# Kernel optimization log

Measured on AMD Instinct MI355X. Metric: run time of the kernel, lower is better.

The kernel has to match this reference:

```python
import jax, jax.numpy as jnp
import numpy as np

# Graph/block sizes: 2-hop sampled minibatch
N0, N1, N2 = 655360, 81920, 8192   # src nodes layer0, dst0/src1, dst1 (seeds)
FAN0, FAN1 = 8, 10
E0, E1 = N1 * FAN0, N2 * FAN1       # 655360, 81920
F_IN, H = 128, 256
BN_EPS = 1e-5
L2_EPS = 1e-12


def setup_inputs() -> dict:
    key = jax.random.key(0)
    ks = jax.random.split(key, 16)
    s = 0.05  # param scale
    inp = {
        "x": jax.random.normal(ks[0], (N0, F_IN), jnp.float32),
        "edge_src0": jax.random.randint(ks[1], (E0,), 0, N0, jnp.int32),
        "edge_dst0": jnp.repeat(jnp.arange(N1, dtype=jnp.int32), FAN0),
        "edge_src1": jax.random.randint(ks[2], (E1,), 0, N1, jnp.int32),
        "edge_dst1": jnp.repeat(jnp.arange(N2, dtype=jnp.int32), FAN1),
        "W_pool0": jax.random.normal(ks[3], (F_IN, F_IN), jnp.float32) * s,
        "b_pool0": jnp.zeros((F_IN,), jnp.float32),
        "W_self0": jax.random.normal(ks[4], (F_IN, H), jnp.float32) * s,
        "W_neigh0": jax.random.normal(ks[5], (F_IN, H), jnp.float32) * s,
        "b0": jnp.zeros((H,), jnp.float32),
        "W_pool1": jax.random.normal(ks[6], (H, H), jnp.float32) * s,
        "b_pool1": jnp.zeros((H,), jnp.float32),
        "W_self1": jax.random.normal(ks[7], (H, H), jnp.float32) * s,
        "W_neigh1": jax.random.normal(ks[8], (H, H), jnp.float32) * s,
        "b1": jnp.zeros((H,), jnp.float32),
        "g_bn0": jnp.ones((H,), jnp.float32),
        "be_bn0": jnp.zeros((H,), jnp.float32),
        "W_h": jax.random.normal(ks[9], (H, H), jnp.float32) * s,
        "b_h": jnp.zeros((H,), jnp.float32),
        "g_bnh": jnp.ones((H,), jnp.float32),
        "be_bnh": jnp.zeros((H,), jnp.float32),
        "W_lat": jax.random.normal(ks[10], (H, H), jnp.float32) * s,
        "b_lat": jnp.zeros((H,), jnp.float32),
        "g_bnl": jnp.ones((H,), jnp.float32),
        "be_bnl": jnp.zeros((H,), jnp.float32),
    }
    return inp


def _sage_pool(h, esrc, edst, n_dst, Wp, bp, Ws, Wn, b):
    # DGL SAGEConv aggregator_type='pool':
    # m = relu(fc_pool(h_src)); pooled[v] = max_{u in N(v)} m[u]
    # out = fc_self(h_dst) + fc_neigh(pooled) + bias
    m = jax.nn.relu(h @ Wp + bp)                                  # [N_src, d]
    pooled = jax.ops.segment_max(m[esrc], edst, num_segments=n_dst)
    return h[:n_dst] @ Ws + pooled @ Wn + b


def _l2norm(h):
    n = jnp.sqrt(jnp.sum(h * h, axis=1, keepdims=True))
    return h / jnp.maximum(n, L2_EPS)


def _bn(h, g, b):
    mu = jnp.mean(h, axis=0)
    var = jnp.var(h, axis=0)
    return (h - mu) * jax.lax.rsqrt(var + BN_EPS) * g + b


def reference(x, edge_src0, edge_dst0, edge_src1, edge_dst1,
              W_pool0, b_pool0, W_self0, W_neigh0, b0,
              W_pool1, b_pool1, W_self1, W_neigh1, b1,
              g_bn0, be_bn0, W_h, b_h, g_bnh, be_bnh,
              W_lat, b_lat, g_bnl, be_bnl):
    # layer 0
    h = _sage_pool(x, edge_src0, edge_dst0, N1, W_pool0, b_pool0, W_self0, W_neigh0, b0)
    h = _l2norm(h)
    h = jax.nn.relu(_bn(h, g_bn0, be_bn0))
    # dropout: eval mode (identity)
    h = jax.nn.relu(_bn(h @ W_h + b_h, g_bnh, be_bnh))   # self.hidden
    # layer 1 (last conv)
    h = _sage_pool(h, edge_src1, edge_dst1, N2, W_pool1, b_pool1, W_self1, W_neigh1, b1)
    h = _l2norm(h)
    # self.latent
    h = _bn(h @ W_lat + b_lat, g_bnl, be_bnl)
    return h
```

## Files before the change

kernel.cpp:

```cpp
#include <hip/hip_runtime.h>

typedef unsigned short u16;
typedef unsigned int u32;
typedef float f32x4 __attribute__((ext_vector_type(4)));
typedef int i32x4 __attribute__((ext_vector_type(4)));
typedef __bf16 bf16x8 __attribute__((ext_vector_type(8)));
typedef short s16x8 __attribute__((ext_vector_type(8)));

#define CN0 655360
#define CN1 81920
#define CN2 8192

#define H0_OFF    0ull
#define T_OFF     41943040ull
#define H2_OFF    83886080ull
#define ZZ_OFF    88080384ull
#define WP0F_OFF  96468992ull
#define WC0F_OFF  96501760ull
#define WHF_OFF   96632832ull
#define WP1F_OFF  96763904ull
#define WC1F_OFF  96894976ull
#define WLATF_OFF 97157120ull
#define STAT_OFF  97288192ull

__device__ inline u16 f2bf(float f) {
  u32 u = __builtin_bit_cast(u32, f);
  return (u16)((u + 0x7fffu + ((u >> 16) & 1u)) >> 16);
}
__device__ inline float bf2f(u16 s) {
  return __builtin_bit_cast(float, (u32)s << 16);
}
__device__ inline i32x4 cvt8(f32x4 a, f32x4 b) {
  union { bf16x8 v; i32x4 q; } u;
  #pragma unroll
  for (int j = 0; j < 4; ++j) { u.v[j] = (__bf16)a[j]; u.v[4 + j] = (__bf16)b[j]; }
  return u.q;
}

template <typename V>
__device__ inline auto mfma_sel(V a, V b, f32x4 c, int)
    -> decltype(__builtin_amdgcn_mfma_f32_16x16x32_bf16(a, b, c, 0, 0, 0)) {
  return __builtin_amdgcn_mfma_f32_16x16x32_bf16(a, b, c, 0, 0, 0);
}
template <typename V>
__device__ inline f32x4 mfma_sel(V a, V b, f32x4 c, long) {
  return __builtin_amdgcn_mfma_f32_16x16x32_bf16(
      __builtin_bit_cast(s16x8, a), __builtin_bit_cast(s16x8, b), c, 0, 0, 0);
}
__device__ inline f32x4 MFMA(i32x4 a, i32x4 b, f32x4 c) {
  return mfma_sel(__builtin_bit_cast(bf16x8, a), __builtin_bit_cast(bf16x8, b), c, 0);
}

__device__ void fragify(const float* W0, const float* W1, int Khalf, int N,
                        u16* dst, int tid, int nthr) {
  int K = W1 ? 2 * Khalf : Khalf;
  int ntile = N >> 4;
  int total = (K >> 5) * ntile * 512;
  for (int i = tid; i < total; i += nthr) {
    int j = i & 7;
    int lane = (i >> 3) & 63;
    int nt = (i >> 9) % ntile;
    int kt = i / (512 * ntile);
    int k = kt * 32 + ((lane >> 4) << 3) + j;
    int n = nt * 16 + (lane & 15);
    float v = (k < Khalf) ? W0[k * N + n] : W1[(k - Khalf) * N + n];
    dst[i] = f2bf(v);
  }
}

__global__ void kprep(const float* Wp0, const float* Ws0, const float* Wn0,
                      const float* Wh, const float* Wp1, const float* Ws1,
                      const float* Wn1, const float* Wlat,
                      u16* wp0f, u16* wc0f, u16* whf, u16* wp1f, u16* wc1f,
                      u16* wlatf, float* stat) {
  int tid = blockIdx.x * blockDim.x + threadIdx.x;
  int nthr = gridDim.x * blockDim.x;
  if (blockIdx.x == 0) {
    #pragma unroll
    for (int i = 0; i < 6; ++i) stat[threadIdx.x + i * 256] = 0.0f;
  }
  fragify(Wp0, nullptr, 128, 128, wp0f, tid, nthr);
  fragify(Ws0, Wn0, 128, 256, wc0f, tid, nthr);
  fragify(Wh, nullptr, 256, 256, whf, tid, nthr);
  fragify(Wp1, nullptr, 256, 256, wp1f, tid, nthr);
  fragify(Ws1, Wn1, 256, 256, wc1f, tid, nthr);
  fragify(Wlat, nullptr, 256, 256, wlatf, tid, nthr);
}

__global__ __launch_bounds__(256, 4)
void k1_layer0(const float* __restrict__ x, const int* __restrict__ esrc,
               const u16* __restrict__ wp0f, const u16* __restrict__ wc0f,
               const float* __restrict__ bp0, const float* __restrict__ b0v,
               u16* __restrict__ h0, float* __restrict__ stat0) {
  __shared__ __align__(16) char lds[16896];
  float* rsb = (float*)(lds + 16384);
  int tid = threadIdx.x, lane = tid & 63, w = tid >> 6;
  int r15 = lane & 15, g = lane >> 4;
  int d0 = blockIdx.x * 32;

  int i_ = tid >> 3, part_ = tid & 7;
  const float* xr_ = x + (size_t)(d0 + i_) * 128 + part_ * 16;
  f32x4 t0 = *(const f32x4*)(xr_ + 0);
  f32x4 t1 = *(const f32x4*)(xr_ + 4);
  f32x4 t2 = *(const f32x4*)(xr_ + 8);
  f32x4 t3 = *(const f32x4*)(xr_ + 12);

  {
    int e0 = d0 * 8 + w * 64;
    const float* rp[4];
    #pragma unroll
    for (int rt = 0; rt < 4; ++rt)
      rp[rt] = x + (size_t)esrc[e0 + rt * 16 + r15] * 128;
    i32x4 afr[4][4];
    #pragma unroll
    for (int rt = 0; rt < 4; ++rt)
      #pragma unroll
      for (int kt = 0; kt < 4; ++kt) {
        f32x4 p0 = *(const f32x4*)(rp[rt] + kt * 32 + g * 8);
        f32x4 p1 = *(const f32x4*)(rp[rt] + kt * 32 + g * 8 + 4);
        afr[rt][kt] = cvt8(p0, p1);
      }
    for (int nt = 0; nt < 8; ++nt) {
      f32x4 acc[4] = {};
      #pragma unroll
      for (int kt = 0; kt < 4; ++kt) {
        i32x4 b = *(const i32x4*)(wp0f + (((kt * 8 + nt) * 64 + lane) << 3));
        #pragma unroll
        for (int rt = 0; rt < 4; ++rt) acc[rt] = MFMA(afr[rt][kt], b, acc[rt]);
      }
      float bias = bp0[nt * 16 + r15];
      #pragma unroll
      for (int rt = 0; rt < 4; ++rt) {
        float mx = fmaxf(fmaxf(acc[rt][0], acc[rt][1]), fmaxf(acc[rt][2], acc[rt][3]));
        mx = fmaxf(mx + bias, 0.0f);
        mx = fmaxf(mx, __shfl_xor(mx, 16));
        if ((g & 1) == 0) {
          u32 row = (u32)(w * 8 + rt * 2 + (g >> 1));
          u32 byte = (row * 512 + 256 + (u32)(nt * 16 + r15) * 2) ^ ((row & 7) << 4);
          *(u16*)(lds + byte) = f2bf(mx);
        }
      }
    }
  }

  {
    u32 sw = (u32)((i_ & 7) << 4);
    *(i32x4*)(lds + (((u32)i_ * 512 + (u32)part_ * 32) ^ sw)) = cvt8(t0, t1);
    *(i32x4*)(lds + (((u32)i_ * 512 + (u32)part_ * 32 + 16) ^ sw)) = cvt8(t2, t3);
  }
  __syncthreads();

  f32x4 acc2[4][2] = {};
  for (int kt = 0; kt < 8; ++kt) {
    u32 r0 = (u32)r15, r1 = (u32)(16 + r15);
    i32x4 a0 = *(const i32x4*)(lds + ((r0 * 512 + (u32)kt * 64 + (u32)g * 16) ^ ((r0 & 7) << 4)));
    i32x4 a1 = *(const i32x4*)(lds + ((r1 * 512 + (u32)kt * 64 + (u32)g * 16) ^ ((r1 & 7) << 4)));
    #pragma unroll
    for (int n4 = 0; n4 < 4; ++n4) {
      int nt = w * 4 + n4;
      i32x4 b = *(const i32x4*)(wc0f + (((size_t)(kt * 16 + nt) * 64 + lane) << 3));
      acc2[n4][0] = MFMA(a0, b, acc2[n4][0]);
      acc2[n4][1] = MFMA(a1, b, acc2[n4][1]);
    }
  }

  float vn[4][2][4];
  #pragma unroll
  for (int n4 = 0; n4 < 4; ++n4) {
    float bv = b0v[(w * 4 + n4) * 16 + r15];
    #pragma unroll
    for (int rt = 0; rt < 2; ++rt)
      #pragma unroll
      for (int j = 0; j < 4; ++j) vn[n4][rt][j] = acc2[n4][rt][j] + bv;
  }
  #pragma unroll
  for (int rt = 0; rt < 2; ++rt)
    #pragma unroll
    for (int j = 0; j < 4; ++j) {
      float s = 0.0f;
      #pragma unroll
      for (int n4 = 0; n4 < 4; ++n4) s += vn[n4][rt][j] * vn[n4][rt][j];
      s += __shfl_xor(s, 1); s += __shfl_xor(s, 2);
      s += __shfl_xor(s, 4); s += __shfl_xor(s, 8);
      if (r15 == 0) rsb[(rt * 16 + g * 4 + j) * 4 + w] = s;
    }
  __syncthreads();

  #pragma unroll
  for (int rt = 0; rt < 2; ++rt)
    #pragma unroll
    for (int j = 0; j < 4; ++j) {
      int r = rt * 16 + g * 4 + j;
      f32x4 q = *(const f32x4*)&rsb[r * 4];
      float rn = 1.0f / fmaxf(sqrtf(q[0] + q[1] + q[2] + q[3]), 1e-12f);
      #pragma unroll
      for (int n4 = 0; n4 < 4; ++n4) vn[n4][rt][j] *= rn;
    }
  #pragma unroll
  for (int n4 = 0; n4 < 4; ++n4) {
    int col = (w * 4 + n4) * 16 + r15;
    float s1 = 0.0f, s2 = 0.0f;
    #pragma unroll
    for (int rt = 0; rt < 2; ++rt)
      #pragma unroll
      for (int j = 0; j < 4; ++j) { float v = vn[n4][rt][j]; s1 += v; s2 += v * v; }
    s1 += __shfl_xor(s1, 16); s1 += __shfl_xor(s1, 32);
    s2 += __shfl_xor(s2, 16); s2 += __shfl_xor(s2, 32);
    if (g == 0) { atomicAdd(&stat0[col], s1); atomicAdd(&stat0[256 + col], s2); }
  }
  #pragma unroll
  for (int n4 = 0; n4 < 4; ++n4)
    #pragma unroll
    for (int rt = 0; rt < 2; ++rt)
      #pragma unroll
      for (int j = 0; j < 4; ++j)
        *(u16*)(lds + (u32)(rt * 16 + g * 4 + j) * 512 + (u32)((w * 4 + n4) * 16 + r15) * 2)
            = f2bf(vn[n4][rt][j]);
  __syncthreads();
  {
    int i = tid >> 3, c8 = tid & 7;
    const char* srcp = lds + i * 512 + c8 * 64;
    u16* dst = h0 + (size_t)(d0 + i) * 256 + c8 * 32;
    #pragma unroll
    for (int c = 0; c < 4; ++c)
      *(i32x4*)(dst + c * 8) = *(const i32x4*)(srcp + c * 16);
  }
}

template <bool RELU_OUT, bool STATS, bool H2OUT>
__global__ __launch_bounds__(256, 4)
void gemm64(const u16* __restrict__ Ain, const float* __restrict__ statin,
            float inv_n, const float* __restrict__ gg, const float* __restrict__ bb,
            const u16* __restrict__ Bf, const float* __restrict__ bias,
            u16* __restrict__ Out, float* __restrict__ statout,
            u16* __restrict__ H2out) {
  __shared__ __align__(16) char lds[34816];
  u16* tb = (u16*)lds;
  float* scs = (float*)(lds + 32768);
  int tid = threadIdx.x, lane = tid & 63, w = tid >> 6;
  int r15 = lane & 15, g = lane >> 4;
  int d0 = blockIdx.x * 64;
  {
    float mu = statin[tid] * inv_n;
    float var = statin[256 + tid] * inv_n - mu * mu;
    float sc = gg[tid] / sqrtf(var + 1e-5f);
    scs[tid] = sc;
    scs[256 + tid] = bb[tid] - mu * sc;
  }
  __syncthreads();

  {
    int i = tid >> 2, part = tid & 3;
    const u16* ar = Ain + (size_t)(d0 + i) * 256 + part * 64;
    u32 sw = (u32)((i & 7) << 4), rowb = (u32)i * 512;
    for (int cc = 0; cc < 8; ++cc) {
      union { i32x4 q; u16 h[8]; } in, out;
      in.q = *(const i32x4*)(ar + cc * 8);
      #pragma unroll
      for (int j = 0; j < 8; ++j) {
        int k = part * 64 + cc * 8 + j;
        float v = fmaxf(bf2f(in.h[j]) * scs[k] + scs[256 + k], 0.0f);
        out.h[j] = f2bf(v);
      }
      *(i32x4*)(lds + ((rowb + (u32)(part * 64 + cc * 8) * 2) ^ sw)) = out.q;
    }
  }
  __syncthreads();

  f32x4 acc[4][4] = {};
  for (int kt = 0; kt < 8; ++kt) {
    i32x4 a[4];
    #pragma unroll
    for (int rt = 0; rt < 4; ++rt) {
      u32 r = (u32)(rt * 16 + r15);
      a[rt] = *(const i32x4*)(lds + ((r * 512 + (u32)kt * 64 + (u32)g * 16) ^ ((r & 7) << 4)));
    }
    #pragma unroll
    for (int n4 = 0; n4 < 4; ++n4) {
      int nt = w * 4 + n4;
      i32x4 b = *(const i32x4*)(Bf + (((size_t)(kt * 16 + nt) * 64 + lane) << 3));
      #pragma unroll
      for (int rt = 0; rt < 4; ++rt) acc[n4][rt] = MFMA(a[rt], b, acc[n4][rt]);
    }
  }
  __syncthreads();

  if constexpr (H2OUT) {
    if (d0 < CN2) {
      int i = tid >> 2, part = tid & 3;
      u16* orow = H2out + (size_t)(d0 + i) * 256 + part * 64;
      u32 sw = (u32)((i & 7) << 4);
      #pragma unroll
      for (int cc = 0; cc < 8; ++cc)
        *(i32x4*)(orow + cc * 8) =
            *(const i32x4*)(lds + (((u32)i * 512 + (u32)(part * 64 + cc * 8) * 2) ^ sw));
    }
    __syncthreads();
  }

  #pragma unroll
  for (int n4 = 0; n4 < 4; ++n4) {
    int col = (w * 4 + n4) * 16 + r15;
    float bv = bias[col];
    #pragma unroll
    for (int rt = 0; rt < 4; ++rt)
      #pragma unroll
      for (int j = 0; j < 4; ++j) {
        float v = acc[n4][rt][j] + bv;
        if (RELU_OUT) v = fmaxf(v, 0.0f);
        tb[(rt * 16 + g * 4 + j) * 256 + col] = f2bf(v);
      }
  }
  __syncthreads();

  {
    int i = tid >> 2, part = tid & 3;
    u16* orow = Out + (size_t)(d0 + i) * 256 + part * 64;
    const u16* trow = tb + i * 256 + part * 64;
    #pragma unroll
    for (int cc = 0; cc < 8; ++cc)
      *(i32x4*)(orow + cc * 8) = *(const i32x4*)(trow + cc * 8);
  }
  if (STATS) {
    int c = tid; float s1 = 0.0f, s2 = 0.0f;
    for (int r = 0; r < 64; ++r) { float v = bf2f(tb[r * 256 + c]); s1 += v; s2 += v * v; }
    atomicAdd(&statout[c], s1); atomicAdd(&statout[256 + c], s2);
  }
}

__global__ __launch_bounds__(256, 4)
void k6_layer1(const int* __restrict__ esrc1, const u16* __restrict__ m1,
               const u16* __restrict__ h2, const u16* __restrict__ wc1f,
               const u16* __restrict__ wlatf, const float* __restrict__ b1v,
               const float* __restrict__ blat, float* __restrict__ zz,
               float* __restrict__ statl) {
  __shared__ __align__(16) char lds[40960];
  float* zbuf = (float*)(lds + 16384);
  int tid = threadIdx.x, lane = tid & 63, w = tid >> 6;
  int r15 = lane & 15, g = lane >> 4;
  int d0 = blockIdx.x * 16;

  {
    int i = tid >> 4, part = tid & 15;
    u32 sw = (u32)((i & 7) << 4);
    const u16* hrow = h2 + (size_t)(d0 + i) * 256 + part * 16;
    i32x4 q0 = *(const i32x4*)(hrow);
    i32x4 q1 = *(const i32x4*)(hrow + 8);
    *(i32x4*)(lds + (((u32)i * 1024 + (u32)(part * 16) * 2) ^ sw)) = q0;
    *(i32x4*)(lds + (((u32)i * 1024 + (u32)(part * 16) * 2 + 16) ^ sw)) = q1;
    float mx[16];
    #pragma unroll
    for (int c = 0; c < 16; ++c) mx[c] = -1e30f;
    const int* ep = esrc1 + (d0 + i) * 10;
    #pragma unroll 2
    for (int e = 0; e < 10; ++e) {
      int src = ep[e];
      const u16* mrow = m1 + (size_t)src * 256 + part * 16;
      union { i32x4 q; u16 h[8]; } a, b;
      a.q = *(const i32x4*)(mrow);
      b.q = *(const i32x4*)(mrow + 8);
      #pragma unroll
      for (int j = 0; j < 8; ++j) {
        mx[j] = fmaxf(mx[j], bf2f(a.h[j]));
        mx[8 + j] = fmaxf(mx[8 + j], bf2f(b.h[j]));
      }
    }
    union { i32x4 q; u16 h[8]; } p0, p1;
    #pragma unroll
    for (int j = 0; j < 8; ++j) { p0.h[j] = f2bf(mx[j]); p1.h[j] = f2bf(mx[8 + j]); }
    *(i32x4*)(lds + (((u32)i * 1024 + (u32)(256 + part * 16) * 2) ^ sw)) = p0.q;
    *(i32x4*)(lds + (((u32)i * 1024 + (u32)(256 + part * 16) * 2 + 16) ^ sw)) = p1.q;
  }
  __syncthreads();

  {
    f32x4 acc[4] = {};
    for (int kt = 0; kt < 16; ++kt) {
      u32 r0 = (u32)r15;
      i32x4 a0 = *(const i32x4*)(lds + ((r0 * 1024 + (u32)kt * 64 + (u32)g * 16) ^ ((r0 & 7) << 4)));
      #pragma unroll
      for (int n4 = 0; n4 < 4; ++n4) {
        int nt = w * 4 + n4;
        i32x4 b = *(const i32x4*)(wc1f + (((size_t)(kt * 16 + nt) * 64 + lane) << 3));
        acc[n4] = MFMA(a0, b, acc[n4]);
      }
    }
    #pragma unroll
    for (int n4 = 0; n4 < 4; ++n4) {
      int col = (w * 4 + n4) * 16 + r15;
      float bv = b1v[col];
      #pragma unroll
      for (int j = 0; j < 4; ++j)
        zbuf[(g * 4 + j) * 256 + col] = acc[n4][j] + bv;
    }
  }
  __syncthreads();

  {
    int i = tid >> 4, part = tid & 15;
    float* zr = zbuf + i * 256 + part * 16;
    f32x4 v0 = *(const f32x4*)(zr + 0), v1 = *(const f32x4*)(zr + 4);
    f32x4 v2 = *(const f32x4*)(zr + 8), v3 = *(const f32x4*)(zr + 12);
    float ss = 0.0f;
    #pragma unroll
    for (int j = 0; j < 4; ++j) ss += v0[j]*v0[j] + v1[j]*v1[j] + v2[j]*v2[j] + v3[j]*v3[j];
    ss += __shfl_xor(ss, 1); ss += __shfl_xor(ss, 2);
    ss += __shfl_xor(ss, 4); ss += __shfl_xor(ss, 8);
    float rn = 1.0f / fmaxf(sqrtf(ss), 1e-12f);
    v0 *= rn; v1 *= rn; v2 *= rn; v3 *= rn;
    u32 sw = (u32)((i & 7) << 4);
    *(i32x4*)(lds + 32768 + (((u32)i * 512 + (u32)(part * 16) * 2) ^ sw)) = cvt8(v0, v1);
    *(i32x4*)(lds + 32768 + (((u32)i * 512 + (u32)(part * 16) * 2 + 16) ^ sw)) = cvt8(v2, v3);
  }
  __syncthreads();

  {
    f32x4 acc[4] = {};
    for (int kt = 0; kt < 8; ++kt) {
      u32 r0 = (u32)r15;
      i32x4 a0 = *(const i32x4*)(lds + 32768 + ((r0 * 512 + (u32)kt * 64 + (u32)g * 16) ^ ((r0 & 7) << 4)));
      #pragma unroll
      for (int n4 = 0; n4 < 4; ++n4) {
        int nt = w * 4 + n4;
        i32x4 b = *(const i32x4*)(wlatf + (((size_t)(kt * 16 + nt) * 64 + lane) << 3));
        acc[n4] = MFMA(a0, b, acc[n4]);
      }
    }
    #pragma unroll
    for (int n4 = 0; n4 < 4; ++n4) {
      int col = (w * 4 + n4) * 16 + r15;
      float bv = blat[col];
      #pragma unroll
      for (int j = 0; j < 4; ++j)
        zbuf[(g * 4 + j) * 256 + col] = acc[n4][j] + bv;
    }
  }
  __syncthreads();

  {
    int i = tid >> 4, part = tid & 15;
    float* zr = zbuf + i * 256 + part * 16;
    float* orow = zz + (size_t)(d0 + i) * 256 + part * 16;
    #pragma unroll
    for (int c = 0; c < 16; c += 4) *(f32x4*)(orow + c) = *(const f32x4*)(zr + c);
  }
  {
    int c = tid; float s1 = 0.0f, s2 = 0.0f;
    #pragma unroll
    for (int r = 0; r < 16; ++r) { float v = zbuf[r * 256 + c]; s1 += v; s2 += v * v; }
    atomicAdd(&statl[c], s1); atomicAdd(&statl[256 + c], s2);
  }
}

__global__ void k7_out(const float* __restrict__ zz, const float* __restrict__ statl,
                       const float* __restrict__ gg, const float* __restrict__ bb,
                       float* __restrict__ out) {
  int idx = blockIdx.x * 256 + threadIdx.x;
  int e0 = idx * 4;
  int c = e0 & 255;
  const float inv_n = 1.0f / (float)CN2;
  f32x4 s1 = *(const f32x4*)(statl + c);
  f32x4 s2 = *(const f32x4*)(statl + 256 + c);
  f32x4 gv = *(const f32x4*)(gg + c);
  f32x4 bv = *(const f32x4*)(bb + c);
  f32x4 v = *(const f32x4*)(zz + e0);
  f32x4 o;
  #pragma unroll
  for (int j = 0; j < 4; ++j) {
    float mu = s1[j] * inv_n;
    float var = s2[j] * inv_n - mu * mu;
    float sc = gv[j] / sqrtf(var + 1e-5f);
    o[j] = v[j] * sc + (bv[j] - mu * sc);
  }
  *(f32x4*)(out + e0) = o;
}

extern "C" void kernel_launch(void* const* d_in, const int* in_sizes, int n_in,
                              void* d_out, int out_size, void* d_ws, size_t ws_size,
                              hipStream_t stream) {
  const float* x     = (const float*)d_in[0];
  const int*   es0   = (const int*)d_in[1];
  const int*   es1   = (const int*)d_in[3];
  const float* Wp0   = (const float*)d_in[5];
  const float* bp0   = (const float*)d_in[6];
  const float* Ws0   = (const float*)d_in[7];
  const float* Wn0   = (const float*)d_in[8];
  const float* b0v   = (const float*)d_in[9];
  const float* Wp1   = (const float*)d_in[10];
  const float* bp1   = (const float*)d_in[11];
  const float* Ws1   = (const float*)d_in[12];
  const float* Wn1   = (const float*)d_in[13];
  const float* b1v   = (const float*)d_in[14];
  const float* gbn0  = (const float*)d_in[15];
  const float* bebn0 = (const float*)d_in[16];
  const float* Wh    = (const float*)d_in[17];
  const float* bh    = (const float*)d_in[18];
  const float* gbnh  = (const float*)d_in[19];
  const float* bebnh = (const float*)d_in[20];
  const float* Wlat  = (const float*)d_in[21];
  const float* blat  = (const float*)d_in[22];
  const float* gbnl  = (const float*)d_in[23];
  const float* bebnl = (const float*)d_in[24];

  char* ws = (char*)d_ws;
  u16* h0    = (u16*)(ws + H0_OFF);
  u16* tban  = (u16*)(ws + T_OFF);
  u16* m1    = (u16*)(ws + H0_OFF);
  u16* h2    = (u16*)(ws + H2_OFF);
  float* zz  = (float*)(ws + ZZ_OFF);
  u16* wp0f  = (u16*)(ws + WP0F_OFF);
  u16* wc0f  = (u16*)(ws + WC0F_OFF);
  u16* whf   = (u16*)(ws + WHF_OFF);
  u16* wp1f  = (u16*)(ws + WP1F_OFF);
  u16* wc1f  = (u16*)(ws + WC1F_OFF);
  u16* wlatf = (u16*)(ws + WLATF_OFF);
  float* stat = (float*)(ws + STAT_OFF);

  kprep<<<64, 256, 0, stream>>>(Wp0, Ws0, Wn0, Wh, Wp1, Ws1, Wn1, Wlat,
                                wp0f, wc0f, whf, wp1f, wc1f, wlatf, stat);
  k1_layer0<<<CN1 / 32, 256, 0, stream>>>(x, es0, wp0f, wc0f, bp0, b0v, h0, stat);
  gemm64<false, true, false><<<CN1 / 64, 256, 0, stream>>>(
      h0, stat, 1.0f / CN1, gbn0, bebn0, whf, bh, tban, stat + 512, nullptr);
  gemm64<true, false, true><<<CN1 / 64, 256, 0, stream>>>(
      tban, stat + 512, 1.0f / CN1, gbnh, bebnh, wp1f, bp1, m1, nullptr, h2);
  k6_layer1<<<CN2 / 16, 256, 0, stream>>>(es1, m1, h2, wc1f, wlatf, b1v, blat, zz,
                                          stat + 1024);
  k7_out<<<out_size / 1024, 256, 0, stream>>>(zz, stat + 1024, gbnl, bebnl,
                                              (float*)d_out);
  (void)in_sizes; (void)n_in; (void)ws_size;
}
```

Measured before the change: 299.5 us.

## Precompute pooled layer-0 messages per source node before gathering

```diff
diff --git a/kernel.cpp b/kernel.cpp
--- a/kernel.cpp
+++ b/kernel.cpp
@@ -22,6 +22,8 @@
 #define WC1F_OFF  96894976ull
 #define WLATF_OFF 97157120ull
 #define STAT_OFF  97288192ull
+#define M_OFF     97294336ull
+#define M_BYTES   167772160ull
 
 __device__ inline u16 f2bf(float f) {
   u32 u = __builtin_bit_cast(u32, f);
@@ -87,6 +89,170 @@
   fragify(Wlat, nullptr, 256, 256, wlatf, tid, nthr);
 }
 
+__global__ __launch_bounds__(256, 6)
+void kM(const float* __restrict__ x, const u16* __restrict__ wp0f,
+        const float* __restrict__ bp0, u16* __restrict__ Mt) {
+  __shared__ __align__(16) u16 mst[64][132];
+  int tid = threadIdx.x, lane = tid & 63, w = tid >> 6;
+  int r15 = lane & 15, g = lane >> 4;
+  size_t row0 = (size_t)blockIdx.x * 64 + (size_t)w * 16;
+  const float* rp = x + (row0 + (size_t)r15) * 128;
+  i32x4 afr[4];
+  #pragma unroll
+  for (int kt = 0; kt < 4; ++kt) {
+    f32x4 p0 = *(const f32x4*)(rp + kt * 32 + g * 8);
+    f32x4 p1 = *(const f32x4*)(rp + kt * 32 + g * 8 + 4);
+    afr[kt] = cvt8(p0, p1);
+  }
+  f32x4 acc[8] = {};
+  #pragma unroll
+  for (int kt = 0; kt < 4; ++kt) {
+    #pragma unroll
+    for (int nt = 0; nt < 8; ++nt) {
+      i32x4 b = *(const i32x4*)(wp0f + (((kt * 8 + nt) * 64 + lane) << 3));
+      acc[nt] = MFMA(afr[kt], b, acc[nt]);
+    }
+  }
+  #pragma unroll
+  for (int nt = 0; nt < 8; ++nt) {
+    float bias = bp0[nt * 16 + r15];
+    #pragma unroll
+    for (int j = 0; j < 4; ++j)
+      mst[w * 16 + g * 4 + j][nt * 16 + r15] = f2bf(fmaxf(acc[nt][j] + bias, 0.0f));
+  }
+  int lr = lane >> 2, lc = lane & 3;
+  u16* orow = Mt + (row0 + (size_t)lr) * 128 + lc * 32;
+  const u16* srow = &mst[w * 16 + lr][lc * 32];
+  #pragma unroll
+  for (int c = 0; c < 4; ++c)
+    *(i32x4*)(orow + c * 8) = *(const i32x4*)(srow + c * 8);
+}
+
+__global__ __launch_bounds__(256, 6)
+void k1b(const u16* __restrict__ Mt, const float* __restrict__ x,
+         const int* __restrict__ esrc, const u16* __restrict__ wc0f,
+         const float* __restrict__ b0v, u16* __restrict__ h0,
+         float* __restrict__ stat0) {
+  __shared__ __align__(16) char lds[16896];
+  float* rsb = (float*)(lds + 16384);
+  int tid = threadIdx.x, lane = tid & 63, w = tid >> 6;
+  int r15 = lane & 15, g = lane >> 4;
+  int d0 = blockIdx.x * 32;
+
+  int i_ = tid >> 3, part_ = tid & 7;
+  const float* xr_ = x + (size_t)(d0 + i_) * 128 + part_ * 16;
+  f32x4 t0 = *(const f32x4*)(xr_ + 0);
+  f32x4 t1 = *(const f32x4*)(xr_ + 4);
+  f32x4 t2 = *(const f32x4*)(xr_ + 8);
+  f32x4 t3 = *(const f32x4*)(xr_ + 12);
+
+  {
+    int i = tid >> 3, part = tid & 7;
+    const int* ep = esrc + (d0 + i) * 8;
+    union { i32x4 q; u16 h[8]; } mx0, mx1;
+    mx0.q = i32x4{0, 0, 0, 0};
+    mx1.q = i32x4{0, 0, 0, 0};
+    #pragma unroll
+    for (int e = 0; e < 8; ++e) {
+      const u16* mr = Mt + (size_t)ep[e] * 128 + part * 16;
+      union { i32x4 q; u16 h[8]; } a, b;
+      a.q = *(const i32x4*)(mr);
+      b.q = *(const i32x4*)(mr + 8);
+      #pragma unroll
+      for (int j = 0; j < 8; ++j) {
+        mx0.h[j] = a.h[j] > mx0.h[j] ? a.h[j] : mx0.h[j];
+        mx1.h[j] = b.h[j] > mx1.h[j] ? b.h[j] : mx1.h[j];
+      }
+    }
+    u32 sw = (u32)((i & 7) << 4);
+    *(i32x4*)(lds + (((u32)i * 512 + 256 + (u32)part * 32) ^ sw)) = mx0.q;
+    *(i32x4*)(lds + (((u32)i * 512 + 256 + (u32)part * 32 + 16) ^ sw)) = mx1.q;
+  }
+
+  {
+    u32 sw = (u32)((i_ & 7) << 4);
+    *(i32x4*)(lds + (((u32)i_ * 512 + (u32)part_ * 32) ^ sw)) = cvt8(t0, t1);
+    *(i32x4*)(lds + (((u32)i_ * 512 + (u32)part_ * 32 + 16) ^ sw)) = cvt8(t2, t3);
+  }
+  __syncthreads();
+
+  f32x4 acc2[4][2] = {};
+  for (int kt = 0; kt < 8; ++kt) {
+    u32 r0 = (u32)r15, r1 = (u32)(16 + r15);
+    i32x4 a0 = *(const i32x4*)(lds + ((r0 * 512 + (u32)kt * 64 + (u32)g * 16) ^ ((r0 & 7) << 4)));
+    i32x4 a1 = *(const i32x4*)(lds + ((r1 * 512 + (u32)kt * 64 + (u32)g * 16) ^ ((r1 & 7) << 4)));
+    #pragma unroll
+    for (int n4 = 0; n4 < 4; ++n4) {
+      int nt = w * 4 + n4;
+      i32x4 b = *(const i32x4*)(wc0f + (((size_t)(kt * 16 + nt) * 64 + lane) << 3));
+      acc2[n4][0] = MFMA(a0, b, acc2[n4][0]);
+      acc2[n4][1] = MFMA(a1, b, acc2[n4][1]);
+    }
+  }
+
+  float vn[4][2][4];
+  #pragma unroll
+  for (int n4 = 0; n4 < 4; ++n4) {
+    float bv = b0v[(w * 4 + n4) * 16 + r15];
+    #pragma unroll
+    for (int rt = 0; rt < 2; ++rt)
+      #pragma unroll
+      for (int j = 0; j < 4; ++j) vn[n4][rt][j] = acc2[n4][rt][j] + bv;
+  }
+  #pragma unroll
+  for (int rt = 0; rt < 2; ++rt)
+    #pragma unroll
+    for (int j = 0; j < 4; ++j) {
+      float s = 0.0f;
+      #pragma unroll
+      for (int n4 = 0; n4 < 4; ++n4) s += vn[n4][rt][j] * vn[n4][rt][j];
+      s += __shfl_xor(s, 1); s += __shfl_xor(s, 2);
+      s += __shfl_xor(s, 4); s += __shfl_xor(s, 8);
+      if (r15 == 0) rsb[(rt * 16 + g * 4 + j) * 4 + w] = s;
+    }
+  __syncthreads();
+
+  #pragma unroll
+  for (int rt = 0; rt < 2; ++rt)
+    #pragma unroll
+    for (int j = 0; j < 4; ++j) {
+      int r = rt * 16 + g * 4 + j;
+      f32x4 q = *(const f32x4*)&rsb[r * 4];
+      float rn = 1.0f / fmaxf(sqrtf(q[0] + q[1] + q[2] + q[3]), 1e-12f);
+      #pragma unroll
+      for (int n4 = 0; n4 < 4; ++n4) vn[n4][rt][j] *= rn;
+    }
+  #pragma unroll
+  for (int n4 = 0; n4 < 4; ++n4) {
+    int col = (w * 4 + n4) * 16 + r15;
+    float s1 = 0.0f, s2 = 0.0f;
+    #pragma unroll
+    for (int rt = 0; rt < 2; ++rt)
+      #pragma unroll
+      for (int j = 0; j < 4; ++j) { float v = vn[n4][rt][j]; s1 += v; s2 += v * v; }
+    s1 += __shfl_xor(s1, 16); s1 += __shfl_xor(s1, 32);
+    s2 += __shfl_xor(s2, 16); s2 += __shfl_xor(s2, 32);
+    if (g == 0) { atomicAdd(&stat0[col], s1); atomicAdd(&stat0[256 + col], s2); }
+  }
+  #pragma unroll
+  for (int n4 = 0; n4 < 4; ++n4)
+    #pragma unroll
+    for (int rt = 0; rt < 2; ++rt)
+      #pragma unroll
+      for (int j = 0; j < 4; ++j)
+        *(u16*)(lds + (u32)(rt * 16 + g * 4 + j) * 512 + (u32)((w * 4 + n4) * 16 + r15) * 2)
+            = f2bf(vn[n4][rt][j]);
+  __syncthreads();
+  {
+    int i = tid >> 3, c8 = tid & 7;
+    const char* srcp = lds + i * 512 + c8 * 64;
+    u16* dst = h0 + (size_t)(d0 + i) * 256 + c8 * 32;
+    #pragma unroll
+    for (int c = 0; c < 4; ++c)
+      *(i32x4*)(dst + c * 8) = *(const i32x4*)(srcp + c * 16);
+  }
+}
+
 __global__ __launch_bounds__(256, 4)
 void k1_layer0(const float* __restrict__ x, const int* __restrict__ esrc,
                const u16* __restrict__ wp0f, const u16* __restrict__ wc0f,
@@ -97,14 +263,12 @@
   int tid = threadIdx.x, lane = tid & 63, w = tid >> 6;
   int r15 = lane & 15, g = lane >> 4;
   int d0 = blockIdx.x * 32;
-
   int i_ = tid >> 3, part_ = tid & 7;
   const float* xr_ = x + (size_t)(d0 + i_) * 128 + part_ * 16;
   f32x4 t0 = *(const f32x4*)(xr_ + 0);
   f32x4 t1 = *(const f32x4*)(xr_ + 4);
   f32x4 t2 = *(const f32x4*)(xr_ + 8);
   f32x4 t3 = *(const f32x4*)(xr_ + 12);
-
   {
     int e0 = d0 * 8 + w * 64;
     const float* rp[4];
@@ -142,14 +306,12 @@
       }
     }
   }
-
   {
     u32 sw = (u32)((i_ & 7) << 4);
     *(i32x4*)(lds + (((u32)i_ * 512 + (u32)part_ * 32) ^ sw)) = cvt8(t0, t1);
     *(i32x4*)(lds + (((u32)i_ * 512 + (u32)part_ * 32 + 16) ^ sw)) = cvt8(t2, t3);
   }
   __syncthreads();
-
   f32x4 acc2[4][2] = {};
   for (int kt = 0; kt < 8; ++kt) {
     u32 r0 = (u32)r15, r1 = (u32)(16 + r15);
@@ -163,7 +325,6 @@
       acc2[n4][1] = MFMA(a1, b, acc2[n4][1]);
     }
   }
-
   float vn[4][2][4];
   #pragma unroll
   for (int n4 = 0; n4 < 4; ++n4) {
@@ -185,7 +346,6 @@
       if (r15 == 0) rsb[(rt * 16 + g * 4 + j) * 4 + w] = s;
     }
   __syncthreads();
-
   #pragma unroll
   for (int rt = 0; rt < 2; ++rt)
     #pragma unroll
@@ -248,7 +408,6 @@
     scs[256 + tid] = bb[tid] - mu * sc;
   }
   __syncthreads();
-
   {
     int i = tid >> 2, part = tid & 3;
     const u16* ar = Ain + (size_t)(d0 + i) * 256 + part * 64;
@@ -339,7 +498,6 @@
   int tid = threadIdx.x, lane = tid & 63, w = tid >> 6;
   int r15 = lane & 15, g = lane >> 4;
   int d0 = blockIdx.x * 16;
-
   {
     int i = tid >> 4, part = tid & 15;
     u32 sw = (u32)((i & 7) << 4);
@@ -372,7 +530,6 @@
     *(i32x4*)(lds + (((u32)i * 1024 + (u32)(256 + part * 16) * 2 + 16) ^ sw)) = p1.q;
   }
   __syncthreads();
-
   {
     f32x4 acc[4] = {};
     for (int kt = 0; kt < 16; ++kt) {
@@ -395,7 +552,6 @@
     }
   }
   __syncthreads();
-
   {
     int i = tid >> 4, part = tid & 15;
     float* zr = zbuf + i * 256 + part * 16;
@@ -413,7 +569,6 @@
     *(i32x4*)(lds + 32768 + (((u32)i * 512 + (u32)(part * 16) * 2 + 16) ^ sw)) = cvt8(v2, v3);
   }
   __syncthreads();
-
   {
     f32x4 acc[4] = {};
     for (int kt = 0; kt < 8; ++kt) {
@@ -436,7 +591,6 @@
     }
   }
   __syncthreads();
-
   {
     int i = tid >> 4, part = tid & 15;
     float* zr = zbuf + i * 256 + part * 16;
@@ -515,10 +669,16 @@
   u16* wc1f  = (u16*)(ws + WC1F_OFF);
   u16* wlatf = (u16*)(ws + WLATF_OFF);
   float* stat = (float*)(ws + STAT_OFF);
+  u16* Mt    = (u16*)(ws + M_OFF);
 
   kprep<<<64, 256, 0, stream>>>(Wp0, Ws0, Wn0, Wh, Wp1, Ws1, Wn1, Wlat,
                                 wp0f, wc0f, whf, wp1f, wc1f, wlatf, stat);
-  k1_layer0<<<CN1 / 32, 256, 0, stream>>>(x, es0, wp0f, wc0f, bp0, b0v, h0, stat);
+  if (ws_size >= M_OFF + M_BYTES) {
+    kM<<<CN0 / 64, 256, 0, stream>>>(x, wp0f, bp0, Mt);
+    k1b<<<CN1 / 32, 256, 0, stream>>>(Mt, x, es0, wc0f, b0v, h0, stat);
+  } else {
+    k1_layer0<<<CN1 / 32, 256, 0, stream>>>(x, es0, wp0f, wc0f, bp0, b0v, h0, stat);
+  }
   gemm64<false, true, false><<<CN1 / 64, 256, 0, stream>>>(
       h0, stat, 1.0f / CN1, gbn0, bebn0, whf, bh, tban, stat + 512, nullptr);
   gemm64<true, false, true><<<CN1 / 64, 256, 0, stream>>>(
@@ -527,5 +687,5 @@
                                           stat + 1024);
   k7_out<<<out_size / 1024, 256, 0, stream>>>(zz, stat + 1024, gbnl, bebnl,
                                               (float*)d_out);
-  (void)in_sizes; (void)n_in; (void)ws_size;
-}
+  (void)in_sizes; (void)n_in;
+}
```

Measured after the change: 383.0 us. 27.9% more time.
